# Kernel optimization log

Measured on AMD Instinct MI355X. Metric: run time of the kernel, lower is better.

## Reference

```python
import jax, jax.numpy as jnp
import numpy as np

B = 4096        # ps.dim_batch
W_ENC = 8192    # ps.width_enc
MAX_LEN = 4096  # max ragged row length


def setup_inputs() -> dict:
    key = jax.random.key(0)
    k1, k2, k3 = jax.random.split(key, 3)
    prev = jax.random.normal(k1, (B, W_ENC), dtype=jnp.float32)
    ragged_vals = jax.random.normal(k2, (B, MAX_LEN), dtype=jnp.float32)
    row_lengths = jax.random.randint(k3, (B,), 0, MAX_LEN, dtype=jnp.int32)
    return {"prev": prev, "ragged_vals": ragged_vals, "row_lengths": row_lengths}


def reference(prev, ragged_vals, row_lengths):
    # Frames.append: concat buffer with new (ragged) frames, then for each
    # row i take the window [lens[i], lens[i] + W_enc) -- a per-row
    # dynamic-offset shift of the streaming buffer.
    w_enc = prev.shape[1]
    y = jnp.concatenate([prev, ragged_vals], axis=1)          # [B, W_enc + max_len]
    cols = jnp.arange(w_enc, dtype=jnp.int32)[None, :] + row_lengths[:, None]  # [B, W_enc]
    y = jnp.take_along_axis(y, cols, axis=1)                  # [B, W_enc]
    lens = row_lengths[:, None]                               # [B, 1]
    return y, lens
```

## Files before the change

kernel.cpp:

```cpp
#include <hip/hip_runtime.h>

constexpr int B       = 4096;
constexpr int W_ENC   = 8192;
constexpr int MAX_LEN = 4096;
constexpr int VPR     = W_ENC / 4;
constexpr int CVPR    = (W_ENC + MAX_LEN) / 4;

__device__ __forceinline__ float4 cvec(const float4* __restrict__ pv,
                                       const float4* __restrict__ rv, int v) {
    const float4* p = (v < VPR) ? (pv + v) : (rv + (v - VPR));
    return *p;
}

__global__ __launch_bounds__(256) void frames_gather_kernel(
        const float* __restrict__ prev,
        const float* __restrict__ ragged,
        const int*   __restrict__ row_lengths,
        float*       __restrict__ out) {
    float* __restrict__ lens_out = out + (size_t)B * W_ENC;

    const int t  = blockIdx.x * blockDim.x + threadIdx.x;
    const int i  = t >> 11;
    const int jv = t & (VPR - 1);
    const int L  = row_lengths[i];

    if (jv == 0) lens_out[i] = (float)L;

    const float4* __restrict__ pv =
        (const float4*)(prev   + (size_t)i * W_ENC);
    const float4* __restrict__ rv =
        (const float4*)(ragged + (size_t)i * MAX_LEN);

    const int q  = L >> 2;
    const int r  = L & 3;
    const int vA = q + jv;

    const float4 A = cvec(pv, rv, vA);
    float4 o;
    if (r == 0) {
        o = A;
    } else {
        const float4 Bv = cvec(pv, rv, vA + 1);
        switch (r) {
        case 1:  o = make_float4(A.y, A.z, A.w, Bv.x); break;
        case 2:  o = make_float4(A.z, A.w, Bv.x, Bv.y); break;
        default: o = make_float4(A.w, Bv.x, Bv.y, Bv.z); break;
        }
    }

    reinterpret_cast<float4*>(out + (size_t)i * W_ENC)[jv] = o;
}

extern "C" void kernel_launch(void* const* d_in, const int* in_sizes, int n_in,
                              void* d_out, int out_size, void* d_ws, size_t ws_size,
                              hipStream_t stream) {
    const float* prev        = (const float*)d_in[0];
    const float* ragged_vals = (const float*)d_in[1];
    const int*   row_lengths = (const int*)d_in[2];
    float*       out         = (float*)d_out;

    const int block = 256;
    const int grid  = (B * VPR) / block;
    frames_gather_kernel<<<grid, block, 0, stream>>>(prev, ragged_vals, row_lengths, out);
}
```

Before: 55.88 us.

## Process one row per block with templated shift and nontemporal stores

Remaps the grid so each 256-thread block handles a whole row, with each thread doing 8 float4 elements that are all loaded before any is stored. The row's shift remainder is resolved once per block through a template switch, which removes per-element branching. Output is written with nontemporal stores to avoid polluting the cache. The grid shrinks sharply, so there are fewer blocks to hide latency but more memory-level parallelism per thread.

```diff
diff --git a/kernel.cpp b/kernel.cpp
--- a/kernel.cpp
+++ b/kernel.cpp
@@ -4,51 +4,66 @@
 constexpr int W_ENC   = 8192;
 constexpr int MAX_LEN = 4096;
 constexpr int VPR     = W_ENC / 4;
-constexpr int CVPR    = (W_ENC + MAX_LEN) / 4;
+constexpr int BLOCK   = 256;
+constexpr int VPT     = VPR / BLOCK;
 
-__device__ __forceinline__ float4 cvec(const float4* __restrict__ pv,
-                                       const float4* __restrict__ rv, int v) {
-    const float4* p = (v < VPR) ? (pv + v) : (rv + (v - VPR));
+typedef float fx4 __attribute__((ext_vector_type(4)));
+
+__device__ __forceinline__ fx4 cvec(const fx4* __restrict__ pv,
+                                    const fx4* __restrict__ rv, int v) {
+    const fx4* p = (v < VPR) ? (pv + v) : (rv + (v - VPR));
     return *p;
 }
 
-__global__ __launch_bounds__(256) void frames_gather_kernel(
+template <int R>
+__device__ __forceinline__ void do_row(const fx4* __restrict__ pv,
+                                       const fx4* __restrict__ rv,
+                                       fx4* __restrict__ ov,
+                                       int q, int tid) {
+    fx4 A[VPT];
+    fx4 Bv[VPT];
+    #pragma unroll
+    for (int m = 0; m < VPT; ++m) {
+        const int vA = q + tid + m * BLOCK;
+        A[m] = cvec(pv, rv, vA);
+        if (R != 0) Bv[m] = cvec(pv, rv, vA + 1);
+    }
+    #pragma unroll
+    for (int m = 0; m < VPT; ++m) {
+        fx4 o;
+        if      (R == 0) o = A[m];
+        else if (R == 1) o = fx4{A[m].y, A[m].z, A[m].w, Bv[m].x};
+        else if (R == 2) o = fx4{A[m].z, A[m].w, Bv[m].x, Bv[m].y};
+        else             o = fx4{A[m].w, Bv[m].x, Bv[m].y, Bv[m].z};
+        __builtin_nontemporal_store(o, ov + tid + m * BLOCK);
+    }
+}
+
+__global__ __launch_bounds__(BLOCK) void frames_gather_kernel(
         const float* __restrict__ prev,
         const float* __restrict__ ragged,
         const int*   __restrict__ row_lengths,
         float*       __restrict__ out) {
-    float* __restrict__ lens_out = out + (size_t)B * W_ENC;
+    const int i = blockIdx.x;
+    const int L = row_lengths[i];
 
-    const int t  = blockIdx.x * blockDim.x + threadIdx.x;
-    const int i  = t >> 11;
-    const int jv = t & (VPR - 1);
-    const int L  = row_lengths[i];
-
-    if (jv == 0) lens_out[i] = (float)L;
-
-    const float4* __restrict__ pv =
-        (const float4*)(prev   + (size_t)i * W_ENC);
-    const float4* __restrict__ rv =
-        (const float4*)(ragged + (size_t)i * MAX_LEN);
-
-    const int q  = L >> 2;
-    const int r  = L & 3;
-    const int vA = q + jv;
-
-    const float4 A = cvec(pv, rv, vA);
-    float4 o;
-    if (r == 0) {
-        o = A;
-    } else {
-        const float4 Bv = cvec(pv, rv, vA + 1);
-        switch (r) {
-        case 1:  o = make_float4(A.y, A.z, A.w, Bv.x); break;
-        case 2:  o = make_float4(A.z, A.w, Bv.x, Bv.y); break;
-        default: o = make_float4(A.w, Bv.x, Bv.y, Bv.z); break;
-        }
+    if (threadIdx.x == 0) {
+        out[(size_t)B * W_ENC + i] = (float)L;
     }
 
-    reinterpret_cast<float4*>(out + (size_t)i * W_ENC)[jv] = o;
+    const fx4* __restrict__ pv = (const fx4*)(prev   + (size_t)i * W_ENC);
+    const fx4* __restrict__ rv = (const fx4*)(ragged + (size_t)i * MAX_LEN);
+    fx4* __restrict__ ov       = (fx4*)(out + (size_t)i * W_ENC);
+
+    const int q   = L >> 2;
+    const int tid = threadIdx.x;
+
+    switch (L & 3) {
+    case 0:  do_row<0>(pv, rv, ov, q, tid); break;
+    case 1:  do_row<1>(pv, rv, ov, q, tid); break;
+    case 2:  do_row<2>(pv, rv, ov, q, tid); break;
+    default: do_row<3>(pv, rv, ov, q, tid); break;
+    }
 }
 
 extern "C" void kernel_launch(void* const* d_in, const int* in_sizes, int n_in,
@@ -59,7 +74,5 @@
     const int*   row_lengths = (const int*)d_in[2];
     float*       out         = (float*)d_out;
 
-    const int block = 256;
-    const int grid  = (B * VPR) / block;
-    frames_gather_kernel<<<grid, block, 0, stream>>>(prev, ragged_vals, row_lengths, out);
+    frames_gather_kernel<<<B, BLOCK, 0, stream>>>(prev, ragged_vals, row_lengths, out);
 }
```

Measured after the change: 44.92 us. 19.6% less time.
